# Optimization experiments

Measured on AMD Instinct MI355X. Metric: run time of the kernel, lower is better.

## Reference

```python
import jax, jax.numpy as jnp
import numpy as np

DIM_Q, DIM_K, DIM_V, H = 256, 256, 384, 6
B, N = 8, 1024
NEG = -10.0 ** 10  # matches torch's (1 - A) * -10**10


def sparsemax(z):
    # simplex projection along last axis (Martins & Astudillo 2016)
    z = z - jnp.max(z, axis=-1, keepdims=True)  # shift-invariant, for fp stability
    z_sorted = jnp.flip(jnp.sort(z, axis=-1), axis=-1)          # descending
    k = jnp.arange(1, z.shape[-1] + 1, dtype=z.dtype)
    z_cumsum = jnp.cumsum(z_sorted, axis=-1)
    support = (1.0 + k * z_sorted) > z_cumsum
    k_z = jnp.sum(support, axis=-1, keepdims=True)              # int32 support size >= 1
    tau = (jnp.take_along_axis(z_cumsum, k_z - 1, axis=-1) - 1.0) / k_z.astype(z.dtype)
    return jnp.maximum(z - tau, 0.0)


def setup_inputs() -> dict:
    key = jax.random.key(0)
    ks = jax.random.split(key, 7)
    Q = jax.random.normal(ks[0], (B, N, DIM_Q), jnp.float32)
    V = jax.random.normal(ks[1], (B, N, DIM_K), jnp.float32)
    # binary adjacency mask with self-loops so every row has support
    A = jax.random.bernoulli(ks[2], 0.05, (B, N, N)).astype(jnp.float32)
    A = A.at[:, jnp.arange(N), jnp.arange(N)].set(1.0)
    # torch.nn.Linear default init: U(-1/sqrt(fan_in), 1/sqrt(fan_in)); weights stored pre-transposed [in, out]
    sq = 1.0 / np.sqrt(DIM_Q)
    sk = 1.0 / np.sqrt(DIM_K)
    WQ = jax.random.uniform(ks[3], (DIM_Q, DIM_V), jnp.float32, -sq, sq)
    bQ = jax.random.uniform(ks[4], (DIM_V,), jnp.float32, -sq, sq)
    WK = jax.random.uniform(ks[5], (DIM_K, DIM_V), jnp.float32, -sk, sk)
    bK = jax.random.uniform(ks[6], (DIM_V,), jnp.float32, -sk, sk)
    return {"Q": Q, "V": V, "A": A, "WQ": WQ, "bQ": bQ, "WK": WK, "bK": bK}


def reference(Q, V, A, WQ, bQ, WK, bK):
    b, n, _ = Q.shape
    d = DIM_V // H
    # project and split heads (torch split along dim=2 == reshape [b,n,H,d])
    q = (Q @ WQ + bQ).reshape(b, n, H, d).transpose(0, 2, 1, 3)   # [b,H,n,d]
    k = (V @ WK + bK).reshape(b, n, H, d).transpose(0, 2, 1, 3)   # [b,H,n,d]
    scale = 1.0 / jnp.sqrt(jnp.float32(DIM_V))
    logits = jnp.einsum('bhnd,bhmd->bhnm', q, k) * scale + (1.0 - A)[:, None] * NEG
    O = sparsemax(logits)                                          # [b,H,n,n], rows on simplex
    # torch: split(B) along dim0 then cat along dim2 -> head-major along last axis
    return O.transpose(0, 2, 1, 3).reshape(b, n, H * n)            # [b,n,H*n]
```

## Files before the change

### kernel.cpp

```cpp
#include <hip/hip_runtime.h>
#include <hip/hip_bf16.h>
#include <stdint.h>

#define DIMK 256
#define DIMV 384
#define NSEQ 1024
#define NHEAD 6
#define ZCAP 192

typedef __attribute__((ext_vector_type(8))) short short8;
typedef __attribute__((ext_vector_type(4))) float floatx4;

__device__ __forceinline__ unsigned short f2b(float f){
  unsigned int x = __float_as_uint(f);
  return (unsigned short)((x + 0x7fffu + ((x >> 16) & 1u)) >> 16);
}
__device__ __forceinline__ unsigned int pack2(float a, float b){
  return (unsigned int)f2b(a) | ((unsigned int)f2b(b) << 16);
}

__global__ __launch_bounds__(256) void fused_pre_kernel(
    const float* __restrict__ Q, const float* __restrict__ V,
    const float* __restrict__ WQ, const float* __restrict__ WK,
    const float* __restrict__ bQ, const float* __restrict__ bK,
    const float* __restrict__ A,
    unsigned short* __restrict__ qf, unsigned short* __restrict__ kf,
    unsigned long long* __restrict__ bm, unsigned short* __restrict__ bmp)
{
  int bid = blockIdx.x;
  if (bid >= 1024){
    int r = (bid - 1024) * 4 + (threadIdx.x >> 6);
    int lane = threadIdx.x & 63;
    const float* arow = A + (size_t)r * NSEQ;
    unsigned long long myw = 0;
    #pragma unroll
    for (int c = 0; c < 16; ++c){
      unsigned long long m = __ballot(arow[c * 64 + lane] > 0.5f);
      if (lane == c) myw = m;
    }
    int own = (lane < 16) ? __popcll(myw) : 0;
    int inc = own;
    #pragma unroll
    for (int o = 1; o < 16; o <<= 1){
      int t = __shfl_up(inc, o, 16);
      if ((lane & 15) >= o) inc += t;
    }
    if (lane < 16){
      bm [(size_t)r * 16 + lane] = myw;
      bmp[(size_t)r * 16 + lane] = (unsigned short)(inc - own);
    }
    return;
  }

  __shared__ uint4 lA[512];
  __shared__ __align__(16) unsigned short lB16[96 * 72];
  int which = bid >> 9;
  int rem = bid & 511;
  int bx = rem >> 2, by = rem & 3;
  const float* X = which ? V : Q;
  const float* W = which ? WK : WQ;
  const float* bias = which ? bK : bQ;

  int t = threadIdx.x;
  int lane = t & 63, wave = t >> 6;
  int wm = wave >> 1, wn = wave & 1;
  int rb = bx * 64;
  int nb = by * 96;
  floatx4 acc[2][3];
  #pragma unroll
  for (int mi = 0; mi < 2; ++mi)
    #pragma unroll
    for (int ni = 0; ni < 3; ++ni) acc[mi][ni] = (floatx4){0.f, 0.f, 0.f, 0.f};

  for (int it = 0; it < 4; ++it){
    int k0 = it * 64;
    #pragma unroll
    for (int i = 0; i < 2; ++i){
      int c = t + i * 256;
      int kc = c >> 6, row = c & 63;
      const float* src = X + (size_t)(rb + row) * DIMK + k0 + kc * 8;
      float4 f0 = *(const float4*)src;
      float4 f1 = *(const float4*)(src + 4);
      uint4 w;
      w.x = pack2(f0.x, f0.y); w.y = pack2(f0.z, f0.w);
      w.z = pack2(f1.x, f1.y); w.w = pack2(f1.z, f1.w);
      lA[c] = w;
    }
    #pragma unroll
    for (int i = 0; i < 6; ++i){
      int c = t + i * 256;
      int kk2 = c / 24, f4 = c % 24;
      float4 wv = *(const float4*)(W + (size_t)(k0 + kk2) * DIMV + nb + f4 * 4);
      int n0 = f4 * 4;
      lB16[(n0    ) * 72 + kk2] = f2b(wv.x);
      lB16[(n0 + 1) * 72 + kk2] = f2b(wv.y);
      lB16[(n0 + 2) * 72 + kk2] = f2b(wv.z);
      lB16[(n0 + 3) * 72 + kk2] = f2b(wv.w);
    }
    __syncthreads();
    #pragma unroll
    for (int kk = 0; kk < 2; ++kk){
      int kc  = kk * 4 + (lane >> 4);
      int r16 = lane & 15;
      short8 af[2], bf[3];
      #pragma unroll
      for (int mi = 0; mi < 2; ++mi)
        af[mi] = *(const short8*)&lA[kc * 64 + wm * 32 + mi * 16 + r16];
      #pragma unroll
      for (int ni = 0; ni < 3; ++ni)
        bf[ni] = *(const short8*)&lB16[(wn * 48 + ni * 16 + r16) * 72 + kc * 8];
      #pragma unroll
      for (int mi = 0; mi < 2; ++mi)
        #pragma unroll
        for (int ni = 0; ni < 3; ++ni)
          acc[mi][ni] = __builtin_amdgcn_mfma_f32_16x16x32_bf16(af[mi], bf[ni], acc[mi][ni], 0, 0, 0);
    }
    __syncthreads();
  }

  const float scale = 0.05103103630798288f;
  unsigned short* lOut = lB16;
  int r16 = lane & 15, rq = lane >> 4;
  #pragma unroll
  for (int ni = 0; ni < 3; ++ni){
    int f   = wn * 48 + ni * 16 + r16;
    int col = nb + f;
    float bv = bias[col];
    int ch = f >> 5;
    int fq = (f >> 3) & 3;
    int d7 = col & 7;
    #pragma unroll
    for (int mi = 0; mi < 2; ++mi){
      int ng = wm * 2 + mi;
      #pragma unroll
      for (int q = 0; q < 4; ++q){
        float v = acc[mi][ni][q] + bv;
        unsigned short o = which ? f2b(v) : f2b(v * scale);
        lOut[ch * 2048 + ng * 512 + fq * 128 + (rq * 4 + q) * 8 + d7] = o;
      }
    }
  }
  __syncthreads();
  int bb = rb >> 10;
  int nb4 = (rb & 1023) >> 4;
  unsigned short* Yd = which ? kf : qf;
  #pragma unroll
  for (int e = 0; e < 3; ++e){
    int col0 = nb + 32 * e;
    int slice = bb * NHEAD + (col0 >> 6);
    int half  = (col0 >> 5) & 1;
    size_t gbase = (((size_t)slice * 2 + half) * 64 + nb4) * 512;
    uint4 vv = *(const uint4*)&lOut[e * 2048 + t * 8];
    *(uint4*)&Yd[gbase + (size_t)t * 8] = vv;
  }
}

__device__ __forceinline__ void red2(float& a, float& b){
  #pragma unroll
  for (int o = 1; o < 64; o <<= 1){ a += __shfl_xor(a, o); b += __shfl_xor(b, o); }
}
__device__ __forceinline__ void red4(float& a, float& b, float& c, float& d){
  #pragma unroll
  for (int o = 1; o < 64; o <<= 1){
    a += __shfl_xor(a, o); b += __shfl_xor(b, o);
    c += __shfl_xor(c, o); d += __shfl_xor(d, o);
  }
}

__global__ __launch_bounds__(512) void attn_kernel(
    const unsigned short* __restrict__ qf, const unsigned short* __restrict__ kf,
    const unsigned long long* __restrict__ bm, const unsigned short* __restrict__ bmp,
    float* __restrict__ out)
{
  __shared__ unsigned long long mw[16][16];
  __shared__ unsigned short    mp[16][16];
  __shared__ float             zlds[16][ZCAP + 1];

  int bid = blockIdx.x;
  int x = bid & 7;
  int u = bid >> 3;
  int h = u >> 6;
  int rb = u & 63;
  int tid = threadIdx.x;
  int lane = tid & 63, w = tid >> 6;
  int slice = x * NHEAD + h;
  int rowbase = (x << 10) + (rb << 4);

  if (tid < 256){
    int rr = tid >> 4, ww = tid & 15;
    mw[rr][ww] = bm [((size_t)(rowbase + rr)) * 16 + ww];
    mp[rr][ww] = bmp[((size_t)(rowbase + rr)) * 16 + ww];
  }

  const short8* qf8 = (const short8*)qf;
  const short8* kf8 = (const short8*)kf;
  size_t ab0 = (((size_t)slice * 2 + 0) * 64 + rb) * 64 + lane;
  size_t ab1 = (((size_t)slice * 2 + 1) * 64 + rb) * 64 + lane;
  short8 ah0 = qf8[ab0];
  short8 ah1 = qf8[ab1];
  __syncthreads();

  __builtin_amdgcn_s_setprio(1);
  #pragma unroll
  for (int i = 0; i < 8; ++i){
    int tt = (w << 3) + i;
    short8 b0 = kf8[(((size_t)slice * 2 + 0) * 64 + tt) * 64 + lane];
    short8 b1 = kf8[(((size_t)slice * 2 + 1) * 64 + tt) * 64 + lane];
    floatx4 a = (floatx4){0.f, 0.f, 0.f, 0.f};
    a = __builtin_amdgcn_mfma_f32_16x16x32_bf16(ah0, b0, a, 0, 0, 0);
    a = __builtin_amdgcn_mfma_f32_16x16x32_bf16(ah1, b1, a, 0, 0, 0);
    int colb = (w << 7) + (i << 4) + (lane & 15);
    int cw = colb >> 6, cb = colb & 63;
    unsigned long long below = (1ull << cb) - 1ull;
    #pragma unroll
    for (int reg = 0; reg < 4; ++reg){
      int rowz = ((lane >> 4) << 2) + reg;
      unsigned long long word = mw[rowz][cw];
      if ((word >> cb) & 1){
        int rank = (int)mp[rowz][cw] + __popcll(word & below);
        if (rank < ZCAP) zlds[rowz][rank] = a[reg];
      }
    }
  }
  __builtin_amdgcn_s_setprio(0);
  __syncthreads();

  int row0 = w * 2, row1 = w * 2 + 1;
  int M0 = (int)mp[row0][15] + __popcll(mw[row0][15]);
  int M1 = (int)mp[row1][15] + __popcll(mw[row1][15]);
  float tau0, tau1;

  if (M0 <= 64 && M1 <= 64){
    bool a0 = lane < M0, a1 = lane < M1;
    float z0 = a0 ? zlds[row0][lane] : 0.f;
    float z1 = a1 ? zlds[row1][lane] : 0.f;
    float s0 = z0, s1 = z1;
    red2(s0, s1);
    tau0 = (s0 - 1.f) / (float)M0;
    tau1 = (s1 - 1.f) / (float)M1;
    int p0 = M0, p1 = M1;
    #pragma unroll 1
    for (int it = 0; it < 32; ++it){
      bool i0 = a0 && z0 > tau0, i1 = a1 && z1 > tau1;
      int n0 = __popcll(__ballot(i0));
      int n1 = __popcll(__ballot(i1));
      s0 = i0 ? z0 : 0.f; s1 = i1 ? z1 : 0.f;
      red2(s0, s1);
      bool stable = (n0 == p0) && (n1 == p1);
      tau0 = (s0 - 1.f) / (float)n0;
      tau1 = (s1 - 1.f) / (float)n1;
      p0 = n0; p1 = n1;
      if (stable) break;
    }
  } else {
    float z0a = (lane < M0)       ? zlds[row0][lane]       : 0.f;
    float z1a = (lane < M1)       ? zlds[row1][lane]       : 0.f;
    float z0b = (64 + lane < M0)  ? zlds[row0][64 + lane]  : 0.f;
    float z1b = (64 + lane < M1)  ? zlds[row1][64 + lane]  : 0.f;
    float z0c = (128 + lane < M0) ? zlds[row0][128 + lane] : 0.f;
    float z1c = (128 + lane < M1) ? zlds[row1][128 + lane] : 0.f;
    bool a0 = lane < M0, b0_ = 64 + lane < M0, c0_ = 128 + lane < M0;
    bool a1 = lane < M1, b1_ = 64 + lane < M1, c1_ = 128 + lane < M1;
    float s0 = (a0 ? z0a : 0.f) + (b0_ ? z0b : 0.f) + (c0_ ? z0c : 0.f);
    float n0 = (a0 ? 1.f : 0.f) + (b0_ ? 1.f : 0.f) + (c0_ ? 1.f : 0.f);
    float s1 = (a1 ? z1a : 0.f) + (b1_ ? z1b : 0.f) + (c1_ ? z1c : 0.f);
    float n1 = (a1 ? 1.f : 0.f) + (b1_ ? 1.f : 0.f) + (c1_ ? 1.f : 0.f);
    red4(s0, n0, s1, n1);
    tau0 = (s0 - 1.f) / n0; tau1 = (s1 - 1.f) / n1;
    float p0 = n0, p1 = n1;
    #pragma unroll 1
    for (int it = 0; it < 32; ++it){
      bool i0a = a0 && z0a > tau0, i0b = b0_ && z0b > tau0, i0c = c0_ && z0c > tau0;
      bool i1a = a1 && z1a > tau1, i1b = b1_ && z1b > tau1, i1c = c1_ && z1c > tau1;
      s0 = (i0a ? z0a : 0.f) + (i0b ? z0b : 0.f) + (i0c ? z0c : 0.f);
      n0 = (i0a ? 1.f : 0.f) + (i0b ? 1.f : 0.f) + (i0c ? 1.f : 0.f);
      s1 = (i1a ? z1a : 0.f) + (i1b ? z1b : 0.f) + (i1c ? z1c : 0.f);
      n1 = (i1a ? 1.f : 0.f) + (i1b ? 1.f : 0.f) + (i1c ? 1.f : 0.f);
      red4(s0, n0, s1, n1);
      bool stable = (n0 == p0) && (n1 == p1);
      tau0 = (s0 - 1.f) / n0; tau1 = (s1 - 1.f) / n1;
      p0 = n0; p1 = n1;
      if (stable) break;
    }
  }

  float* o0 = out + ((size_t)(rowbase + row0) * NHEAD + h) * NSEQ;
  float* o1 = out + ((size_t)(rowbase + row1) * NHEAD + h) * NSEQ;
  int b0v = (lane & 15) << 2;
  unsigned long long pmask = (1ull << b0v) - 1ull;
  #pragma unroll
  for (int qtr = 0; qtr < 4; ++qtr){
    int cw = (qtr << 2) + (lane >> 4);
    unsigned long long w0 = mw[row0][cw], w1 = mw[row1][cw];
    int rk0 = (int)mp[row0][cw] + __popcll(w0 & pmask);
    int rk1 = (int)mp[row1][cw] + __popcll(w1 & pmask);
    float v0[4], v1[4];
    #pragma unroll
    for (int j = 0; j < 4; ++j){
      int bit0 = (int)((w0 >> (b0v + j)) & 1ull);
      int bit1 = (int)((w1 >> (b0v + j)) & 1ull);
      v0[j] = bit0 ? fmaxf(zlds[row0][rk0] - tau0, 0.f) : 0.f;
      v1[j] = bit1 ? fmaxf(zlds[row1][rk1] - tau1, 0.f) : 0.f;
      rk0 += bit0; rk1 += bit1;
    }
    ((float4*)o0)[(qtr << 6) + lane] = make_float4(v0[0], v0[1], v0[2], v0[3]);
    ((float4*)o1)[(qtr << 6) + lane] = make_float4(v1[0], v1[1], v1[2], v1[3]);
  }
}

extern "C" void kernel_launch(void* const* d_in, const int* in_sizes, int n_in,
                              void* d_out, int out_size, void* d_ws, size_t ws_size,
                              hipStream_t stream) {
  const float* Q  = (const float*)d_in[0];
  const float* V  = (const float*)d_in[1];
  const float* A  = (const float*)d_in[2];
  const float* WQ = (const float*)d_in[3];
  const float* bQ = (const float*)d_in[4];
  const float* WK = (const float*)d_in[5];
  const float* bK = (const float*)d_in[6];
  float* out = (float*)d_out;

  char* ws = (char*)d_ws;
  unsigned short*     qf  = (unsigned short*)ws;
  unsigned short*     kf  = (unsigned short*)(ws + (size_t)6291456);
  unsigned long long* bm  = (unsigned long long*)(ws + (size_t)12582912);
  unsigned short*     bmp = (unsigned short*)(ws + (size_t)13631488);
  (void)in_sizes; (void)n_in; (void)out_size; (void)ws_size;

  fused_pre_kernel<<<3072, 256, 0, stream>>>(Q, V, WQ, WK, bQ, bK, A,
                                             qf, kf, bm, bmp);
  attn_kernel<<<3072, 512, 0, stream>>>(qf, kf, bm, bmp, out);
}
```

Baseline: 81.66 us.

## Process 32 query rows per attention block to reuse K fragments

Each attention block now handles two 16-row query groups instead of one. Every K fragment loaded from global memory feeds two MFMA chains, which halves K traffic per output row, and the grid shrinks from 3072 to 1536 blocks. The sparsemax and output phase runs two passes per wave, each over two rows. LDS use roughly doubles and each block's serial work grows, which can lower occupancy and latency hiding.

```diff
diff --git a/kernel.cpp b/kernel.cpp
--- a/kernel.cpp
+++ b/kernel.cpp
@@ -172,21 +172,21 @@
     const unsigned long long* __restrict__ bm, const unsigned short* __restrict__ bmp,
     float* __restrict__ out)
 {
-  __shared__ unsigned long long mw[16][16];
-  __shared__ unsigned short    mp[16][16];
-  __shared__ float             zlds[16][ZCAP + 1];
+  __shared__ unsigned long long mw[32][16];
+  __shared__ unsigned short    mp[32][16];
+  __shared__ float             zlds[32][ZCAP + 1];
 
   int bid = blockIdx.x;
   int x = bid & 7;
   int u = bid >> 3;
-  int h = u >> 6;
-  int rb = u & 63;
+  int h = u >> 5;
+  int rblk = u & 31;
   int tid = threadIdx.x;
   int lane = tid & 63, w = tid >> 6;
   int slice = x * NHEAD + h;
-  int rowbase = (x << 10) + (rb << 4);
-
-  if (tid < 256){
+  int rowbase = (x << 10) + (rblk << 5);
+
+  {
     int rr = tid >> 4, ww = tid & 15;
     mw[rr][ww] = bm [((size_t)(rowbase + rr)) * 16 + ww];
     mp[rr][ww] = bmp[((size_t)(rowbase + rr)) * 16 + ww];
@@ -194,10 +194,13 @@
 
   const short8* qf8 = (const short8*)qf;
   const short8* kf8 = (const short8*)kf;
-  size_t ab0 = (((size_t)slice * 2 + 0) * 64 + rb) * 64 + lane;
-  size_t ab1 = (((size_t)slice * 2 + 1) * 64 + rb) * 64 + lane;
-  short8 ah0 = qf8[ab0];
-  short8 ah1 = qf8[ab1];
+  int ng0 = (rblk << 1), ng1 = ng0 + 1;
+  size_t a00 = (((size_t)slice * 2 + 0) * 64 + ng0) * 64 + lane;
+  size_t a01 = (((size_t)slice * 2 + 1) * 64 + ng0) * 64 + lane;
+  size_t a10 = (((size_t)slice * 2 + 0) * 64 + ng1) * 64 + lane;
+  size_t a11 = (((size_t)slice * 2 + 1) * 64 + ng1) * 64 + lane;
+  short8 q00 = qf8[a00], q01 = qf8[a01];
+  short8 q10 = qf8[a10], q11 = qf8[a11];
   __syncthreads();
 
   __builtin_amdgcn_s_setprio(1);
@@ -206,105 +209,116 @@
     int tt = (w << 3) + i;
     short8 b0 = kf8[(((size_t)slice * 2 + 0) * 64 + tt) * 64 + lane];
     short8 b1 = kf8[(((size_t)slice * 2 + 1) * 64 + tt) * 64 + lane];
-    floatx4 a = (floatx4){0.f, 0.f, 0.f, 0.f};
-    a = __builtin_amdgcn_mfma_f32_16x16x32_bf16(ah0, b0, a, 0, 0, 0);
-    a = __builtin_amdgcn_mfma_f32_16x16x32_bf16(ah1, b1, a, 0, 0, 0);
+    floatx4 a0 = (floatx4){0.f, 0.f, 0.f, 0.f};
+    floatx4 a1 = (floatx4){0.f, 0.f, 0.f, 0.f};
+    a0 = __builtin_amdgcn_mfma_f32_16x16x32_bf16(q00, b0, a0, 0, 0, 0);
+    a0 = __builtin_amdgcn_mfma_f32_16x16x32_bf16(q01, b1, a0, 0, 0, 0);
+    a1 = __builtin_amdgcn_mfma_f32_16x16x32_bf16(q10, b0, a1, 0, 0, 0);
+    a1 = __builtin_amdgcn_mfma_f32_16x16x32_bf16(q11, b1, a1, 0, 0, 0);
     int colb = (w << 7) + (i << 4) + (lane & 15);
     int cw = colb >> 6, cb = colb & 63;
     unsigned long long below = (1ull << cb) - 1ull;
     #pragma unroll
     for (int reg = 0; reg < 4; ++reg){
       int rowz = ((lane >> 4) << 2) + reg;
-      unsigned long long word = mw[rowz][cw];
-      if ((word >> cb) & 1){
-        int rank = (int)mp[rowz][cw] + __popcll(word & below);
-        if (rank < ZCAP) zlds[rowz][rank] = a[reg];
+      unsigned long long w0 = mw[rowz][cw];
+      if ((w0 >> cb) & 1){
+        int rank = (int)mp[rowz][cw] + __popcll(w0 & below);
+        if (rank < ZCAP) zlds[rowz][rank] = a0[reg];
+      }
+      unsigned long long w1 = mw[16 + rowz][cw];
+      if ((w1 >> cb) & 1){
+        int rank = (int)mp[16 + rowz][cw] + __popcll(w1 & below);
+        if (rank < ZCAP) zlds[16 + rowz][rank] = a1[reg];
       }
     }
   }
   __builtin_amdgcn_s_setprio(0);
   __syncthreads();
 
-  int row0 = w * 2, row1 = w * 2 + 1;
-  int M0 = (int)mp[row0][15] + __popcll(mw[row0][15]);
-  int M1 = (int)mp[row1][15] + __popcll(mw[row1][15]);
-  float tau0, tau1;
-
-  if (M0 <= 64 && M1 <= 64){
-    bool a0 = lane < M0, a1 = lane < M1;
-    float z0 = a0 ? zlds[row0][lane] : 0.f;
-    float z1 = a1 ? zlds[row1][lane] : 0.f;
-    float s0 = z0, s1 = z1;
-    red2(s0, s1);
-    tau0 = (s0 - 1.f) / (float)M0;
-    tau1 = (s1 - 1.f) / (float)M1;
-    int p0 = M0, p1 = M1;
-    #pragma unroll 1
-    for (int it = 0; it < 32; ++it){
-      bool i0 = a0 && z0 > tau0, i1 = a1 && z1 > tau1;
-      int n0 = __popcll(__ballot(i0));
-      int n1 = __popcll(__ballot(i1));
-      s0 = i0 ? z0 : 0.f; s1 = i1 ? z1 : 0.f;
+  #pragma unroll 1
+  for (int pass = 0; pass < 2; ++pass){
+    int row0 = (w << 2) + (pass << 1), row1 = row0 + 1;
+    int M0 = (int)mp[row0][15] + __popcll(mw[row0][15]);
+    int M1 = (int)mp[row1][15] + __popcll(mw[row1][15]);
+    float tau0, tau1;
+
+    if (M0 <= 64 && M1 <= 64){
+      bool a0 = lane < M0, a1 = lane < M1;
+      float z0 = a0 ? zlds[row0][lane] : 0.f;
+      float z1 = a1 ? zlds[row1][lane] : 0.f;
+      float s0 = z0, s1 = z1;
       red2(s0, s1);
-      bool stable = (n0 == p0) && (n1 == p1);
-      tau0 = (s0 - 1.f) / (float)n0;
-      tau1 = (s1 - 1.f) / (float)n1;
-      p0 = n0; p1 = n1;
-      if (stable) break;
-    }
-  } else {
-    float z0a = (lane < M0)       ? zlds[row0][lane]       : 0.f;
-    float z1a = (lane < M1)       ? zlds[row1][lane]       : 0.f;
-    float z0b = (64 + lane < M0)  ? zlds[row0][64 + lane]  : 0.f;
-    float z1b = (64 + lane < M1)  ? zlds[row1][64 + lane]  : 0.f;
-    float z0c = (128 + lane < M0) ? zlds[row0][128 + lane] : 0.f;
-    float z1c = (128 + lane < M1) ? zlds[row1][128 + lane] : 0.f;
-    bool a0 = lane < M0, b0_ = 64 + lane < M0, c0_ = 128 + lane < M0;
-    bool a1 = lane < M1, b1_ = 64 + lane < M1, c1_ = 128 + lane < M1;
-    float s0 = (a0 ? z0a : 0.f) + (b0_ ? z0b : 0.f) + (c0_ ? z0c : 0.f);
-    float n0 = (a0 ? 1.f : 0.f) + (b0_ ? 1.f : 0.f) + (c0_ ? 1.f : 0.f);
-    float s1 = (a1 ? z1a : 0.f) + (b1_ ? z1b : 0.f) + (c1_ ? z1c : 0.f);
-    float n1 = (a1 ? 1.f : 0.f) + (b1_ ? 1.f : 0.f) + (c1_ ? 1.f : 0.f);
-    red4(s0, n0, s1, n1);
-    tau0 = (s0 - 1.f) / n0; tau1 = (s1 - 1.f) / n1;
-    float p0 = n0, p1 = n1;
-    #pragma unroll 1
-    for (int it = 0; it < 32; ++it){
-      bool i0a = a0 && z0a > tau0, i0b = b0_ && z0b > tau0, i0c = c0_ && z0c > tau0;
-      bool i1a = a1 && z1a > tau1, i1b = b1_ && z1b > tau1, i1c = c1_ && z1c > tau1;
-      s0 = (i0a ? z0a : 0.f) + (i0b ? z0b : 0.f) + (i0c ? z0c : 0.f);
-      n0 = (i0a ? 1.f : 0.f) + (i0b ? 1.f : 0.f) + (i0c ? 1.f : 0.f);
-      s1 = (i1a ? z1a : 0.f) + (i1b ? z1b : 0.f) + (i1c ? z1c : 0.f);
-      n1 = (i1a ? 1.f : 0.f) + (i1b ? 1.f : 0.f) + (i1c ? 1.f : 0.f);
+      tau0 = (s0 - 1.f) / (float)M0;
+      tau1 = (s1 - 1.f) / (float)M1;
+      int p0 = M0, p1 = M1;
+      #pragma unroll 1
+      for (int it = 0; it < 32; ++it){
+        bool i0 = a0 && z0 > tau0, i1 = a1 && z1 > tau1;
+        int n0 = __popcll(__ballot(i0));
+        int n1 = __popcll(__ballot(i1));
+        s0 = i0 ? z0 : 0.f; s1 = i1 ? z1 : 0.f;
+        red2(s0, s1);
+        bool stable = (n0 == p0) && (n1 == p1);
+        tau0 = (s0 - 1.f) / (float)n0;
+        tau1 = (s1 - 1.f) / (float)n1;
+        p0 = n0; p1 = n1;
+        if (stable) break;
+      }
+    } else {
+      float z0a = (lane < M0)       ? zlds[row0][lane]       : 0.f;
+      float z1a = (lane < M1)       ? zlds[row1][lane]       : 0.f;
+      float z0b = (64 + lane < M0)  ? zlds[row0][64 + lane]  : 0.f;
+      float z1b = (64 + lane < M1)  ? zlds[row1][64 + lane]  : 0.f;
+      float z0c = (128 + lane < M0) ? zlds[row0][128 + lane] : 0.f;
+      float z1c = (128 + lane < M1) ? zlds[row1][128 + lane] : 0.f;
+      bool a0 = lane < M0, b0_ = 64 + lane < M0, c0_ = 128 + lane < M0;
+      bool a1 = lane < M1, b1_ = 64 + lane < M1, c1_ = 128 + lane < M1;
+      float s0 = (a0 ? z0a : 0.f) + (b0_ ? z0b : 0.f) + (c0_ ? z0c : 0.f);
+      float n0 = (a0 ? 1.f : 0.f) + (b0_ ? 1.f : 0.f) + (c0_ ? 1.f : 0.f);
+      float s1 = (a1 ? z1a : 0.f) + (b1_ ? z1b : 0.f) + (c1_ ? z1c : 0.f);
+      float n1 = (a1 ? 1.f : 0.f) + (b1_ ? 1.f : 0.f) + (c1_ ? 1.f : 0.f);
       red4(s0, n0, s1, n1);
-      bool stable = (n0 == p0) && (n1 == p1);
       tau0 = (s0 - 1.f) / n0; tau1 = (s1 - 1.f) / n1;
-      p0 = n0; p1 = n1;
-      if (stable) break;
-    }
-  }
-
-  float* o0 = out + ((size_t)(rowbase + row0) * NHEAD + h) * NSEQ;
-  float* o1 = out + ((size_t)(rowbase + row1) * NHEAD + h) * NSEQ;
-  int b0v = (lane & 15) << 2;
-  unsigned long long pmask = (1ull << b0v) - 1ull;
-  #pragma unroll
-  for (int qtr = 0; qtr < 4; ++qtr){
-    int cw = (qtr << 2) + (lane >> 4);
-    unsigned long long w0 = mw[row0][cw], w1 = mw[row1][cw];
-    int rk0 = (int)mp[row0][cw] + __popcll(w0 & pmask);
-    int rk1 = (int)mp[row1][cw] + __popcll(w1 & pmask);
-    float v0[4], v1[4];
-    #pragma unroll
-    for (int j = 0; j < 4; ++j){
-      int bit0 = (int)((w0 >> (b0v + j)) & 1ull);
-      int bit1 = (int)((w1 >> (b0v + j)) & 1ull);
-      v0[j] = bit0 ? fmaxf(zlds[row0][rk0] - tau0, 0.f) : 0.f;
-      v1[j] = bit1 ? fmaxf(zlds[row1][rk1] - tau1, 0.f) : 0.f;
-      rk0 += bit0; rk1 += bit1;
-    }
-    ((float4*)o0)[(qtr << 6) + lane] = make_float4(v0[0], v0[1], v0[2], v0[3]);
-    ((float4*)o1)[(qtr << 6) + lane] = make_float4(v1[0], v1[1], v1[2], v1[3]);
+      float p0 = n0, p1 = n1;
+      #pragma unroll 1
+      for (int it = 0; it < 32; ++it){
+        bool i0a = a0 && z0a > tau0, i0b = b0_ && z0b > tau0, i0c = c0_ && z0c > tau0;
+        bool i1a = a1 && z1a > tau1, i1b = b1_ && z1b > tau1, i1c = c1_ && z1c > tau1;
+        s0 = (i0a ? z0a : 0.f) + (i0b ? z0b : 0.f) + (i0c ? z0c : 0.f);
+        n0 = (i0a ? 1.f : 0.f) + (i0b ? 1.f : 0.f) + (i0c ? 1.f : 0.f);
+        s1 = (i1a ? z1a : 0.f) + (i1b ? z1b : 0.f) + (i1c ? z1c : 0.f);
+        n1 = (i1a ? 1.f : 0.f) + (i1b ? 1.f : 0.f) + (i1c ? 1.f : 0.f);
+        red4(s0, n0, s1, n1);
+        bool stable = (n0 == p0) && (n1 == p1);
+        tau0 = (s0 - 1.f) / n0; tau1 = (s1 - 1.f) / n1;
+        p0 = n0; p1 = n1;
+        if (stable) break;
+      }
+    }
+
+    float* o0 = out + ((size_t)(rowbase + row0) * NHEAD + h) * NSEQ;
+    float* o1 = out + ((size_t)(rowbase + row1) * NHEAD + h) * NSEQ;
+    int b0v = (lane & 15) << 2;
+    unsigned long long pmask = (1ull << b0v) - 1ull;
+    #pragma unroll
+    for (int qtr = 0; qtr < 4; ++qtr){
+      int cw = (qtr << 2) + (lane >> 4);
+      unsigned long long w0 = mw[row0][cw], w1 = mw[row1][cw];
+      int rk0 = (int)mp[row0][cw] + __popcll(w0 & pmask);
+      int rk1 = (int)mp[row1][cw] + __popcll(w1 & pmask);
+      float v0[4], v1[4];
+      #pragma unroll
+      for (int j = 0; j < 4; ++j){
+        int bit0 = (int)((w0 >> (b0v + j)) & 1ull);
+        int bit1 = (int)((w1 >> (b0v + j)) & 1ull);
+        v0[j] = bit0 ? fmaxf(zlds[row0][rk0] - tau0, 0.f) : 0.f;
+        v1[j] = bit1 ? fmaxf(zlds[row1][rk1] - tau1, 0.f) : 0.f;
+        rk0 += bit0; rk1 += bit1;
+      }
+      ((float4*)o0)[(qtr << 6) + lane] = make_float4(v0[0], v0[1], v0[2], v0[3]);
+      ((float4*)o1)[(qtr << 6) + lane] = make_float4(v1[0], v1[1], v1[2], v1[3]);
+    }
   }
 }
 
@@ -329,5 +343,5 @@
 
   fused_pre_kernel<<<3072, 256, 0, stream>>>(Q, V, WQ, WK, bQ, bK, A,
                                              qf, kf, bm, bmp);
-  attn_kernel<<<3072, 512, 0, stream>>>(qf, kf, bm, bmp, out);
-}
+  attn_kernel<<<1536, 512, 0, stream>>>(qf, kf, bm, bmp, out);
+}
```

After: 83.59 us. 2.4% more time.
